# Optimization experiments

Measured on AMD Instinct MI355X. Metric: run time of the kernel, lower is better.

## Reference

```python
import jax, jax.numpy as jnp
import numpy as np

# Model dims
T = 256        # seq_length (timesteps)
B = 16384      # batch
IN = 1024      # hardcoded input feature dim of LILinearCell
C = 10         # n_classes
# norse LIParameters defaults
DT = 1e-3
TAU_SYN_INV = 200.0
TAU_MEM_INV = 100.0
V_LEAK = 0.0


def setup_inputs() -> dict:
    key = jax.random.key(0)
    kx, kw = jax.random.split(key)
    x = jax.random.normal(kx, (B, IN), dtype=jnp.float32)
    # LILinearCell weight init: randn(out,in) * sqrt(2/in)
    W = jax.random.normal(kw, (C, IN), dtype=jnp.float32) * np.float32(np.sqrt(2.0 / IN))
    return {"x": x, "W": W}


def reference(x, W):
    # uses_ts=False: the same x feeds every timestep, so the synaptic input
    # current x @ W^T is constant across the scan.
    xW = x @ W.T  # [B, C]

    def step(state, _):
        v, i = state
        # norse li_step:
        i_jump = i + xW
        v_new = v + DT * TAU_MEM_INV * ((V_LEAK - v) + i_jump)
        i_new = i_jump - DT * TAU_SYN_INV * i_jump
        return (v_new, i_new), v_new

    v0 = jnp.full((x.shape[0], W.shape[0]), V_LEAK, dtype=x.dtype)
    i0 = jnp.zeros((x.shape[0], W.shape[0]), dtype=x.dtype)
    _, voltages = jax.lax.scan(step, (v0, i0), None, length=T)
    return voltages  # [T, B, C]
```

## Files before the change

kernel.cpp:

```cpp
#include <hip/hip_runtime.h>

#define T_STEPS 256
#define B_ROWS  16384
#define IN_DIM  1024
#define C_CLS   10

typedef float vfloat4 __attribute__((ext_vector_type(4)));

__global__ __launch_bounds__(256) void gemv_kernel(
    const float4* __restrict__ x4,
    const float4* __restrict__ W4,
    float* __restrict__ xw)
{
    const int wave = threadIdx.x >> 6;
    const int lane = threadIdx.x & 63;
    const int row_base = blockIdx.x * 16 + wave * 4;

    float acc[4][C_CLS];
#pragma unroll
    for (int r = 0; r < 4; ++r)
#pragma unroll
        for (int c = 0; c < C_CLS; ++c) acc[r][c] = 0.0f;

#pragma unroll
    for (int p = 0; p < 4; ++p) {
        float4 w[C_CLS];
#pragma unroll
        for (int c = 0; c < C_CLS; ++c)
            w[c] = W4[c * 256 + p * 64 + lane];

#pragma unroll
        for (int r = 0; r < 4; ++r) {
            float4 xv = x4[(size_t)(row_base + r) * 256 + p * 64 + lane];
#pragma unroll
            for (int c = 0; c < C_CLS; ++c) {
                acc[r][c] = fmaf(xv.x, w[c].x,
                            fmaf(xv.y, w[c].y,
                            fmaf(xv.z, w[c].z,
                            fmaf(xv.w, w[c].w, acc[r][c]))));
            }
        }
    }

#pragma unroll
    for (int r = 0; r < 4; ++r)
#pragma unroll
        for (int c = 0; c < C_CLS; ++c) {
            float v = acc[r][c];
#pragma unroll
            for (int off = 32; off >= 1; off >>= 1)
                v += __shfl_xor(v, off, 64);
            acc[r][c] = v;
        }

    if (lane == 0) {
#pragma unroll
        for (int r = 0; r < 4; ++r)
#pragma unroll
            for (int c = 0; c < C_CLS; ++c)
                xw[(row_base + r) * C_CLS + c] = acc[r][c];
    }
}

__global__ __launch_bounds__(256) void expand_kernel(
    const float4* __restrict__ xw4,
    float4* __restrict__ out4)
{
    const int SLICE4 = (B_ROWS * C_CLS) / 4;
    const int TOTAL4 = T_STEPS * SLICE4;
    const float L9 = -0.15200309344504995f;
    const float L8 = -0.32192809488736235f;

    int idx = blockIdx.x * blockDim.x + threadIdx.x;
    const int stride = gridDim.x * blockDim.x;
    for (; idx < TOTAL4; idx += stride) {
        int t  = idx / SLICE4;
        int r4 = idx - t * SLICE4;
        float t1 = (float)(t + 1);
        float coef = 5.0f - 9.0f * exp2f(t1 * L9) + 4.0f * exp2f(t1 * L8);
        float4 v = xw4[r4];
        vfloat4 o;
        o.x = v.x * coef; o.y = v.y * coef; o.z = v.z * coef; o.w = v.w * coef;
        __builtin_nontemporal_store(o, (vfloat4*)(out4 + idx));
    }
}

extern "C" void kernel_launch(void* const* d_in, const int* in_sizes, int n_in,
                              void* d_out, int out_size, void* d_ws, size_t ws_size,
                              hipStream_t stream) {
    const float* x = (const float*)d_in[0];
    const float* W = (const float*)d_in[1];
    float* out = (float*)d_out;
    float* xw  = (float*)d_ws;

    gemv_kernel<<<B_ROWS / 16, 256, 0, stream>>>(
        (const float4*)x, (const float4*)W, xw);

    expand_kernel<<<2048, 256, 0, stream>>>(
        (const float4*)xw, (float4*)out);
}
```

Baseline: 224.4 us.

## Restructure GEMV lane mapping and chunk time steps in expand kernel

The GEMV now assigns 16 lanes per row, so each row needs only a 4-step shuffle reduction, and W is reloaded per class inside the loop rather than held in registers. The expand kernel drops the grid-stride loop with its per-element division and exp2 calls. Each thread now loads its xw value once and writes 16 consecutive timesteps, updating the coefficient powers by multiplying by 0.9 and 0.8 each step. This cuts integer and transcendental work, but the recurrence may drift slightly in rounding and the GEMV issues more W loads.

```diff
diff --git a/kernel.cpp b/kernel.cpp
--- a/kernel.cpp
+++ b/kernel.cpp
@@ -12,76 +12,78 @@
     const float4* __restrict__ W4,
     float* __restrict__ xw)
 {
-    const int wave = threadIdx.x >> 6;
-    const int lane = threadIdx.x & 63;
-    const int row_base = blockIdx.x * 16 + wave * 4;
+    const int tid  = threadIdx.x;
+    const int wave = tid >> 6;
+    const int lane = tid & 63;
+    const int sub  = lane >> 4;
+    const int ql   = lane & 15;
+    const int row  = blockIdx.x * 16 + wave * 4 + sub;
 
-    float acc[4][C_CLS];
+    float acc[C_CLS];
 #pragma unroll
-    for (int r = 0; r < 4; ++r)
+    for (int c = 0; c < C_CLS; ++c) acc[c] = 0.0f;
+
+    const float4* __restrict__ xrow = x4 + (size_t)row * 256;
+
+#pragma unroll 4
+    for (int p = 0; p < 16; ++p) {
+        float4 xv = xrow[p * 16 + ql];
 #pragma unroll
-        for (int c = 0; c < C_CLS; ++c) acc[r][c] = 0.0f;
-
-#pragma unroll
-    for (int p = 0; p < 4; ++p) {
-        float4 w[C_CLS];
-#pragma unroll
-        for (int c = 0; c < C_CLS; ++c)
-            w[c] = W4[c * 256 + p * 64 + lane];
-
-#pragma unroll
-        for (int r = 0; r < 4; ++r) {
-            float4 xv = x4[(size_t)(row_base + r) * 256 + p * 64 + lane];
-#pragma unroll
-            for (int c = 0; c < C_CLS; ++c) {
-                acc[r][c] = fmaf(xv.x, w[c].x,
-                            fmaf(xv.y, w[c].y,
-                            fmaf(xv.z, w[c].z,
-                            fmaf(xv.w, w[c].w, acc[r][c]))));
-            }
+        for (int c = 0; c < C_CLS; ++c) {
+            float4 w = W4[c * 256 + p * 16 + ql];
+            acc[c] = fmaf(xv.x, w.x,
+                     fmaf(xv.y, w.y,
+                     fmaf(xv.z, w.z,
+                     fmaf(xv.w, w.w, acc[c]))));
         }
     }
 
 #pragma unroll
-    for (int r = 0; r < 4; ++r)
+    for (int c = 0; c < C_CLS; ++c) {
+        float v = acc[c];
 #pragma unroll
-        for (int c = 0; c < C_CLS; ++c) {
-            float v = acc[r][c];
+        for (int off = 8; off >= 1; off >>= 1)
+            v += __shfl_xor(v, off, 64);
+        acc[c] = v;
+    }
+
+    if (ql == 0) {
 #pragma unroll
-            for (int off = 32; off >= 1; off >>= 1)
-                v += __shfl_xor(v, off, 64);
-            acc[r][c] = v;
-        }
-
-    if (lane == 0) {
-#pragma unroll
-        for (int r = 0; r < 4; ++r)
-#pragma unroll
-            for (int c = 0; c < C_CLS; ++c)
-                xw[(row_base + r) * C_CLS + c] = acc[r][c];
+        for (int c = 0; c < C_CLS; ++c)
+            xw[row * C_CLS + c] = acc[c];
     }
 }
 
+#define T_CHUNK 16
 __global__ __launch_bounds__(256) void expand_kernel(
     const float4* __restrict__ xw4,
     float4* __restrict__ out4)
 {
     const int SLICE4 = (B_ROWS * C_CLS) / 4;
-    const int TOTAL4 = T_STEPS * SLICE4;
+    const int NR     = SLICE4 / 256;
+
+    const int rblk = blockIdx.x % NR;
+    const int tblk = blockIdx.x / NR;
+    const int r4   = rblk * 256 + threadIdx.x;
+    const int t0   = tblk * T_CHUNK;
+
     const float L9 = -0.15200309344504995f;
     const float L8 = -0.32192809488736235f;
 
-    int idx = blockIdx.x * blockDim.x + threadIdx.x;
-    const int stride = gridDim.x * blockDim.x;
-    for (; idx < TOTAL4; idx += stride) {
-        int t  = idx / SLICE4;
-        int r4 = idx - t * SLICE4;
-        float t1 = (float)(t + 1);
-        float coef = 5.0f - 9.0f * exp2f(t1 * L9) + 4.0f * exp2f(t1 * L8);
-        float4 v = xw4[r4];
+    float4 v = xw4[r4];
+    float p9 = exp2f((float)(t0 + 1) * L9);
+    float p8 = exp2f((float)(t0 + 1) * L8);
+
+    float4* dst = out4 + (size_t)t0 * SLICE4 + r4;
+#pragma unroll
+    for (int i = 0; i < T_CHUNK; ++i) {
+        float coef = fmaf(-9.0f, p9, fmaf(4.0f, p8, 5.0f));
         vfloat4 o;
         o.x = v.x * coef; o.y = v.y * coef; o.z = v.z * coef; o.w = v.w * coef;
-        __builtin_nontemporal_store(o, (vfloat4*)(out4 + idx));
+        __builtin_nontemporal_store(o, (vfloat4*)dst);
+        dst += SLICE4;
+        p9 *= 0.9f;
+        p8 *= 0.8f;
     }
 }
 
@@ -96,6 +98,6 @@
     gemv_kernel<<<B_ROWS / 16, 256, 0, stream>>>(
         (const float4*)x, (const float4*)W, xw);
 
-    expand_kernel<<<2048, 256, 0, stream>>>(
+    expand_kernel<<<(T_STEPS / T_CHUNK) * ((B_ROWS * C_CLS) / 4 / 256), 256, 0, stream>>>(
         (const float4*)xw, (float4*)out);
 }
```

After: 233.1 us. +3.9%, slower.

## Fuse GEMV and timestep expansion into a single kernel via shared memory

Applied to the files above, without the earlier changes.

Merges the GEMV and the output expansion into one kernel. Each block reduces its 16 rows of xW into shared memory, then writes the 256-timestep scaled output for those rows directly. The cross-lane reduction is restructured so each 16-lane group finishes one row, which cuts the number of shuffles. This removes the second launch and the workspace round trip. In exchange, the output stores become strided: each block writes 640 bytes per timestep, spread across 256 timesteps.

```diff
diff --git a/kernel.cpp b/kernel.cpp
--- a/kernel.cpp
+++ b/kernel.cpp
@@ -7,13 +7,17 @@
 
 typedef float vfloat4 __attribute__((ext_vector_type(4)));
 
-__global__ __launch_bounds__(256) void gemv_kernel(
+__global__ __launch_bounds__(256) void fused_kernel(
     const float4* __restrict__ x4,
     const float4* __restrict__ W4,
-    float* __restrict__ xw)
+    float4* __restrict__ out4)
 {
-    const int wave = threadIdx.x >> 6;
-    const int lane = threadIdx.x & 63;
+    __shared__ __align__(16) float sm[16 * C_CLS];
+
+    const int tid  = threadIdx.x;
+    const int wave = tid >> 6;
+    const int lane = tid & 63;
+    const int sub  = lane >> 4;
     const int row_base = blockIdx.x * 16 + wave * 4;
 
     float acc[4][C_CLS];
@@ -43,45 +47,49 @@
     }
 
 #pragma unroll
-    for (int r = 0; r < 4; ++r)
+    for (int c = 0; c < C_CLS; ++c) {
 #pragma unroll
-        for (int c = 0; c < C_CLS; ++c) {
-            float v = acc[r][c];
+        for (int r = 0; r < 4; ++r) {
+            acc[r][c] += __shfl_xor(acc[r][c], 32, 64);
+            acc[r][c] += __shfl_xor(acc[r][c], 16, 64);
+        }
+        float p = (sub < 2) ? (sub == 0 ? acc[0][c] : acc[1][c])
+                            : (sub == 2 ? acc[2][c] : acc[3][c]);
+        p += __shfl_xor(p, 8, 64);
+        p += __shfl_xor(p, 4, 64);
+        p += __shfl_xor(p, 2, 64);
+        p += __shfl_xor(p, 1, 64);
+        if ((lane & 15) == 0)
+            sm[(wave * 4 + sub) * C_CLS + c] = p;
+    }
+    __syncthreads();
+
+    const float4* sm4 = (const float4*)sm;
+    float4 xwf[C_CLS];
 #pragma unroll
-            for (int off = 32; off >= 1; off >>= 1)
-                v += __shfl_xor(v, off, 64);
-            acc[r][c] = v;
-        }
+    for (int j = 0; j < C_CLS; ++j)
+        xwf[j] = sm4[(tid & 3) + 4 * j];
 
-    if (lane == 0) {
-#pragma unroll
-        for (int r = 0; r < 4; ++r)
-#pragma unroll
-            for (int c = 0; c < C_CLS; ++c)
-                xw[(row_base + r) * C_CLS + c] = acc[r][c];
-    }
-}
-
-__global__ __launch_bounds__(256) void expand_kernel(
-    const float4* __restrict__ xw4,
-    float4* __restrict__ out4)
-{
-    const int SLICE4 = (B_ROWS * C_CLS) / 4;
-    const int TOTAL4 = T_STEPS * SLICE4;
     const float L9 = -0.15200309344504995f;
     const float L8 = -0.32192809488736235f;
+    const int   SLICE4 = (B_ROWS * C_CLS) / 4;
+    const size_t col = (size_t)blockIdx.x * 40 + (tid & 3);
+    const int tq = tid >> 2;
 
-    int idx = blockIdx.x * blockDim.x + threadIdx.x;
-    const int stride = gridDim.x * blockDim.x;
-    for (; idx < TOTAL4; idx += stride) {
-        int t  = idx / SLICE4;
-        int r4 = idx - t * SLICE4;
-        float t1 = (float)(t + 1);
-        float coef = 5.0f - 9.0f * exp2f(t1 * L9) + 4.0f * exp2f(t1 * L8);
-        float4 v = xw4[r4];
-        vfloat4 o;
-        o.x = v.x * coef; o.y = v.y * coef; o.z = v.z * coef; o.w = v.w * coef;
-        __builtin_nontemporal_store(o, (vfloat4*)(out4 + idx));
+#pragma unroll
+    for (int tc = 0; tc < 4; ++tc) {
+        const int t = tc * 64 + tq;
+        const float t1 = (float)(t + 1);
+        const float coef = fmaf(-9.0f, exp2f(t1 * L9),
+                           fmaf(4.0f, exp2f(t1 * L8), 5.0f));
+        float4* dst = out4 + (size_t)t * SLICE4 + col;
+#pragma unroll
+        for (int j = 0; j < C_CLS; ++j) {
+            vfloat4 o;
+            o.x = xwf[j].x * coef; o.y = xwf[j].y * coef;
+            o.z = xwf[j].z * coef; o.w = xwf[j].w * coef;
+            __builtin_nontemporal_store(o, (vfloat4*)(dst + 4 * j));
+        }
     }
 }
 
@@ -91,11 +99,7 @@
     const float* x = (const float*)d_in[0];
     const float* W = (const float*)d_in[1];
     float* out = (float*)d_out;
-    float* xw  = (float*)d_ws;
 
-    gemv_kernel<<<B_ROWS / 16, 256, 0, stream>>>(
-        (const float4*)x, (const float4*)W, xw);
-
-    expand_kernel<<<2048, 256, 0, stream>>>(
-        (const float4*)xw, (float4*)out);
+    fused_kernel<<<B_ROWS / 16, 256, 0, stream>>>(
+        (const float4*)x, (const float4*)W, (float4*)out);
 }
```

After: 244.3 us. 1.09x slower.
